# Kernel optimization log

Measured on AMD Instinct MI355X. Metric: run time of the kernel, lower is better.

## Reference

```python
import jax, jax.numpy as jnp
import numpy as np

B, T, D, S = 4, 8192, 512, 16

def setup_inputs() -> dict:
    key = jax.random.key(0)
    k1, k2, k3, k4, k5 = jax.random.split(key, 5)
    x = jax.random.normal(k1, (B, T, D), dtype=jnp.float32)
    # splat parameters as in __init__: centers ~ 0.02*randn, log_scales = 0
    centers = jax.random.normal(k2, (S, D), dtype=jnp.float32) * 0.02
    log_scales = jnp.zeros((S,), dtype=jnp.float32)
    # xavier-uniform linear weights (gain = 1/(1+layer_idx*0.1) = 1.0 for layer 0)
    limit = float(np.sqrt(6.0 / (D + D)))
    Wv = jax.random.uniform(k3, (D, D), minval=-limit, maxval=limit, dtype=jnp.float32)
    Wo = jax.random.uniform(k4, (D, D), minval=-limit, maxval=limit, dtype=jnp.float32)
    return {"x": x, "centers": centers, "log_scales": log_scales, "Wv": Wv, "Wo": Wo}

def reference(x, centers, log_scales, Wv, Wo):
    # scales clamped as in EnhancedAdaptiveSplat.get_scale
    scales = jnp.clip(jnp.exp(log_scales), 0.1, 2.0)           # [S]
    v = jnp.einsum('btd,ed->bte', x, Wv)                       # value projection [B,T,D]
    # squared distance token<->splat via expansion (no [B,T,S,D] intermediate)
    x2 = jnp.sum(x * x, axis=-1, keepdims=True)                # [B,T,1]
    c2 = jnp.sum(centers * centers, axis=-1)                   # [S]
    xc = jnp.einsum('btd,sd->bts', x, centers)                 # [B,T,S]
    d2 = x2 + c2 - 2.0 * xc                                    # [B,T,S]
    logits = -0.5 * d2 / (scales * scales)                     # gaussian kernel log-weights
    attn = jax.nn.softmax(logits, axis=-1)                     # normalize over splats [B,T,S]
    # tokens -> splats aggregation, then splats -> tokens distribution
    splat_states = jnp.einsum('bts,btd->bsd', attn, v)         # [B,S,D]
    out = jnp.einsum('bts,bsd->btd', attn, splat_states)       # [B,T,D]
    return jnp.einsum('btd,ed->bte', out, Wo)                  # output projection
```

## Files before the change

### kernel.cpp

```cpp
#include <hip/hip_runtime.h>
#include <hip/hip_bf16.h>
#include <math.h>

#define B_ 4
#define T_ 8192
#define D_ 512
#define S_ 16

#define CHUNK 64


typedef __attribute__((ext_vector_type(8))) short bf16x8;
typedef __attribute__((ext_vector_type(4))) float f32x4;

__device__ __forceinline__ float dot4(float4 a, float4 b) {
  return a.x * b.x + a.y * b.y + a.z * b.z + a.w * b.w;
}

__device__ __forceinline__ bf16x8 pack8(float4 a, float4 b) {
  union { __hip_bfloat162 h[4]; bf16x8 v; } u;
  u.h[0] = __float22bfloat162_rn(make_float2(a.x, a.y));
  u.h[1] = __float22bfloat162_rn(make_float2(a.z, a.w));
  u.h[2] = __float22bfloat162_rn(make_float2(b.x, b.y));
  u.h[3] = __float22bfloat162_rn(make_float2(b.z, b.w));
  return u.v;
}

__global__ __launch_bounds__(256, 2) void attn_ts_k(const float* __restrict__ x,
                                                    const float* __restrict__ centers,
                                                    const float* __restrict__ log_scales,
                                                    float* __restrict__ attn,
                                                    float* __restrict__ ts) {
  __shared__ __align__(16) float a_s[CHUNK][S_];
  const int lane = threadIdx.x & 63;
  const int w = threadIdx.x >> 6;
  const int g = lane >> 4;
  const int n = lane & 15;
  const int b = blockIdx.x >> 7;
  const int t0 = (blockIdx.x & 127) * CHUNK;
  const int tw = t0 + (w << 4);

  {
    bf16x8 cf[16];
    float c2p = 0.f;
    const float* crow = centers + n * D_ + (g << 3);
#pragma unroll
    for (int st = 0; st < 16; ++st) {
      float4 c0 = *(const float4*)(crow + st * 32);
      float4 c1 = *(const float4*)(crow + st * 32 + 4);
      c2p += dot4(c0, c0) + dot4(c1, c1);
      cf[st] = pack8(c0, c1);
    }
    c2p += __shfl_xor(c2p, 16, 64);
    c2p += __shfl_xor(c2p, 32, 64);

    const float sc = fminf(fmaxf(__expf(log_scales[n]), 0.1f), 2.0f);
    const float inv2 = 0.5f / (sc * sc);

    const float* xrow = x + ((size_t)b * T_ + tw + n) * D_ + (g << 3);
    f32x4 acc = {0.f, 0.f, 0.f, 0.f};
    float x2p = 0.f;
#pragma unroll
    for (int st = 0; st < 16; ++st) {
      float4 x0 = *(const float4*)(xrow + st * 32);
      float4 x1 = *(const float4*)(xrow + st * 32 + 4);
      x2p += dot4(x0, x0) + dot4(x1, x1);
      acc = __builtin_amdgcn_mfma_f32_16x16x32_bf16(pack8(x0, x1), cf[st], acc,
                                                    0, 0, 0);
    }
    x2p += __shfl_xor(x2p, 16, 64);
    x2p += __shfl_xor(x2p, 32, 64);

    float lg[4];
#pragma unroll
    for (int r = 0; r < 4; ++r) {
      float x2r = __shfl(x2p, (lane & 48) | ((g << 2) + r), 64);
      lg[r] = (2.f * acc[r] - x2r - c2p) * inv2;
    }

    float mx[4] = {lg[0], lg[1], lg[2], lg[3]};
#pragma unroll
    for (int dlt = 1; dlt < 16; dlt <<= 1)
#pragma unroll
      for (int r = 0; r < 4; ++r) mx[r] = fmaxf(mx[r], __shfl_xor(mx[r], dlt, 64));
    float ev[4], sm[4];
#pragma unroll
    for (int r = 0; r < 4; ++r) { ev[r] = __expf(lg[r] - mx[r]); sm[r] = ev[r]; }
#pragma unroll
    for (int dlt = 1; dlt < 16; dlt <<= 1)
#pragma unroll
      for (int r = 0; r < 4; ++r) sm[r] += __shfl_xor(sm[r], dlt, 64);

    float* ar = attn + ((size_t)b * T_ + tw) * S_;
#pragma unroll
    for (int r = 0; r < 4; ++r) {
      float av = ev[r] / sm[r];
      int trow = (g << 2) + r;
      ar[trow * S_ + n] = av;
      a_s[(w << 4) + trow][n] = av;
    }
  }

  __syncthreads();

  {
    const int d = threadIdx.x;
    float2 acc[S_];
#pragma unroll
    for (int si = 0; si < S_; ++si) acc[si] = make_float2(0.f, 0.f);

    const float* xb = x + ((size_t)b * T_ + t0) * D_;

#pragma unroll 8
    for (int t = 0; t < CHUNK; ++t) {
      float xv0 = xb[(size_t)t * D_ + d];
      float xv1 = xb[(size_t)t * D_ + d + 256];
      const float4* ap = (const float4*)a_s[t];
      float4 q0 = ap[0], q1 = ap[1], q2 = ap[2], q3 = ap[3];
      float av[S_] = {q0.x, q0.y, q0.z, q0.w, q1.x, q1.y, q1.z, q1.w,
                      q2.x, q2.y, q2.z, q2.w, q3.x, q3.y, q3.z, q3.w};
#pragma unroll
      for (int si = 0; si < S_; ++si) {
        acc[si].x += av[si] * xv0;
        acc[si].y += av[si] * xv1;
      }
    }

    float* tb = ts + (size_t)b * S_ * D_;
#pragma unroll
    for (int si = 0; si < S_; ++si) {
      atomicAdd(tb + si * D_ + d, acc[si].x);
      atomicAdd(tb + si * D_ + d + 256, acc[si].y);
    }
  }
}

__global__ __launch_bounds__(256) void proj_k(const float* __restrict__ in,
                                              const float* __restrict__ W,
                                              float* __restrict__ out) {
  __shared__ float red[4][64];
  const int r = blockIdx.x >> 3;
  const int eb = blockIdx.x & 7;
  const int el = threadIdx.x & 63;
  const int kc = threadIdx.x >> 6;
  const int e = (eb << 6) + el;

  const float4* w4 = (const float4*)(W + (size_t)e * D_ + kc * 128);
  const float4* i4 = (const float4*)(in + (size_t)r * D_ + kc * 128);
  float acc = 0.f;
#pragma unroll
  for (int k = 0; k < 32; ++k) acc += dot4(w4[k], i4[k]);

  red[kc][el] = acc;
  __syncthreads();
  if (kc == 0)
    out[(size_t)r * D_ + e] = red[0][el] + red[1][el] + red[2][el] + red[3][el];
}

#define K4_TOK 64
__global__ __launch_bounds__(256) void out_k(const float* __restrict__ attn,
                                             const float* __restrict__ ss_o,
                                             float* __restrict__ out) {
  const int chunks = T_ / K4_TOK;
  const int b = blockIdx.x / chunks;
  const int t0 = (blockIdx.x % chunks) * K4_TOK;
  const int w = threadIdx.x >> 6;
  const int lane = threadIdx.x & 63;
  const int e0 = (w << 7) + (lane << 1);

  float2 ssf[S_];
  const float* sb = ss_o + (size_t)b * S_ * D_;
#pragma unroll
  for (int s = 0; s < S_; ++s) ssf[s] = *(const float2*)(sb + s * D_ + e0);

  const float4* ab = (const float4*)(attn + ((size_t)b * T_ + t0) * S_);
  float* ob = out + ((size_t)b * T_ + t0) * D_ + e0;

#pragma unroll 4
  for (int t = 0; t < K4_TOK; ++t) {
    float4 a0 = ab[t * 4 + 0], a1 = ab[t * 4 + 1];
    float4 a2 = ab[t * 4 + 2], a3 = ab[t * 4 + 3];
    float av[S_] = {a0.x, a0.y, a0.z, a0.w, a1.x, a1.y, a1.z, a1.w,
                    a2.x, a2.y, a2.z, a2.w, a3.x, a3.y, a3.z, a3.w};
    float2 acc = make_float2(0.f, 0.f);
#pragma unroll
    for (int s = 0; s < S_; ++s) {
      acc.x += av[s] * ssf[s].x;
      acc.y += av[s] * ssf[s].y;
    }
    *(float2*)(ob + (size_t)t * D_) = acc;
  }
}

extern "C" void kernel_launch(void* const* d_in, const int* in_sizes, int n_in,
                              void* d_out, int out_size, void* d_ws, size_t ws_size,
                              hipStream_t stream) {
  const float* x          = (const float*)d_in[0];
  const float* centers    = (const float*)d_in[1];
  const float* log_scales = (const float*)d_in[2];
  const float* Wv         = (const float*)d_in[3];
  const float* Wo         = (const float*)d_in[4];
  float* out = (float*)d_out;

  float* attn = (float*)d_ws;
  float* ts   = attn + (size_t)B_ * T_ * S_;
  float* tmp  = ts + (size_t)B_ * S_ * D_;
  float* ss_o = tmp + (size_t)B_ * S_ * D_;

  hipMemsetAsync(ts, 0, (size_t)B_ * S_ * D_ * sizeof(float), stream);

  attn_ts_k<<<B_ * (T_ / CHUNK), 256, 0, stream>>>(x, centers, log_scales, attn, ts);
  proj_k<<<512, 256, 0, stream>>>(ts, Wv, tmp);
  proj_k<<<512, 256, 0, stream>>>(tmp, Wo, ss_o);
  out_k<<<B_ * (T_ / K4_TOK), 256, 0, stream>>>(attn, ss_o, out);
}
```

Measured before the change: 179.5 us.

## Halve token chunk, split D across wave pairs with LDS reduction

Token chunk per block drops from 64 to 32, doubling the grid of attn_ts_k and out_k. In attn_ts_k each 16-token tile is now computed by two waves, each covering half of D, and their MFMA partial sums plus norm partials are combined through shared memory before the softmax. Occupancy target rises to 4 blocks per SM. The aim is more parallelism and lower register pressure (no 16-entry cached center fragment), at the cost of an extra barrier, LDS traffic, idle waves during the softmax, and twice as many atomicAdds into ts.

```diff
diff --git a/kernel.cpp b/kernel.cpp
--- a/kernel.cpp
+++ b/kernel.cpp
@@ -7,7 +7,7 @@
 #define D_ 512
 #define S_ 16
 
-#define CHUNK 64
+#define CHUNK 32
 
 
 typedef __attribute__((ext_vector_type(8))) short bf16x8;
@@ -26,56 +26,69 @@
   return u.v;
 }
 
-__global__ __launch_bounds__(256, 2) void attn_ts_k(const float* __restrict__ x,
+__global__ __launch_bounds__(256, 4) void attn_ts_k(const float* __restrict__ x,
                                                     const float* __restrict__ centers,
                                                     const float* __restrict__ log_scales,
                                                     float* __restrict__ attn,
                                                     float* __restrict__ ts) {
   __shared__ __align__(16) float a_s[CHUNK][S_];
-  const int lane = threadIdx.x & 63;
-  const int w = threadIdx.x >> 6;
+  __shared__ float red[6][4][64];
+  const int tid = threadIdx.x;
+  const int lane = tid & 63;
+  const int w = tid >> 6;
   const int g = lane >> 4;
   const int n = lane & 15;
-  const int b = blockIdx.x >> 7;
-  const int t0 = (blockIdx.x & 127) * CHUNK;
-  const int tw = t0 + (w << 4);
+  const int b = blockIdx.x >> 8;
+  const int t0 = (blockIdx.x & 255) * CHUNK;
+  const int pair = w & 1;
+  const int half = w >> 1;
+  const int tw = t0 + (pair << 4);
 
   {
-    bf16x8 cf[16];
-    float c2p = 0.f;
-    const float* crow = centers + n * D_ + (g << 3);
-#pragma unroll
-    for (int st = 0; st < 16; ++st) {
+    const float* crow = centers + n * D_ + (half << 8) + (g << 3);
+    const float* xrow = x + ((size_t)b * T_ + tw + n) * D_ + (half << 8) + (g << 3);
+    f32x4 acc = {0.f, 0.f, 0.f, 0.f};
+    float x2p = 0.f, c2p = 0.f;
+#pragma unroll
+    for (int st = 0; st < 8; ++st) {
+      float4 x0 = *(const float4*)(xrow + st * 32);
+      float4 x1 = *(const float4*)(xrow + st * 32 + 4);
       float4 c0 = *(const float4*)(crow + st * 32);
       float4 c1 = *(const float4*)(crow + st * 32 + 4);
+      x2p += dot4(x0, x0) + dot4(x1, x1);
       c2p += dot4(c0, c0) + dot4(c1, c1);
-      cf[st] = pack8(c0, c1);
-    }
+      acc = __builtin_amdgcn_mfma_f32_16x16x32_bf16(pack8(x0, x1), pack8(c0, c1),
+                                                    acc, 0, 0, 0);
+    }
+    x2p += __shfl_xor(x2p, 16, 64);
+    x2p += __shfl_xor(x2p, 32, 64);
     c2p += __shfl_xor(c2p, 16, 64);
     c2p += __shfl_xor(c2p, 32, 64);
 
+    red[0][w][lane] = acc[0];
+    red[1][w][lane] = acc[1];
+    red[2][w][lane] = acc[2];
+    red[3][w][lane] = acc[3];
+    red[4][w][lane] = x2p;
+    red[5][w][lane] = c2p;
+  }
+  __syncthreads();
+
+  if (w < 2) {
+    float accr[4];
+#pragma unroll
+    for (int r = 0; r < 4; ++r) accr[r] = red[r][w][lane] + red[r][w + 2][lane];
+    float x2 = red[4][w][lane] + red[4][w + 2][lane];
+    float c2 = red[5][w][lane] + red[5][w + 2][lane];
+
     const float sc = fminf(fmaxf(__expf(log_scales[n]), 0.1f), 2.0f);
     const float inv2 = 0.5f / (sc * sc);
 
-    const float* xrow = x + ((size_t)b * T_ + tw + n) * D_ + (g << 3);
-    f32x4 acc = {0.f, 0.f, 0.f, 0.f};
-    float x2p = 0.f;
-#pragma unroll
-    for (int st = 0; st < 16; ++st) {
-      float4 x0 = *(const float4*)(xrow + st * 32);
-      float4 x1 = *(const float4*)(xrow + st * 32 + 4);
-      x2p += dot4(x0, x0) + dot4(x1, x1);
-      acc = __builtin_amdgcn_mfma_f32_16x16x32_bf16(pack8(x0, x1), cf[st], acc,
-                                                    0, 0, 0);
-    }
-    x2p += __shfl_xor(x2p, 16, 64);
-    x2p += __shfl_xor(x2p, 32, 64);
-
     float lg[4];
 #pragma unroll
     for (int r = 0; r < 4; ++r) {
-      float x2r = __shfl(x2p, (lane & 48) | ((g << 2) + r), 64);
-      lg[r] = (2.f * acc[r] - x2r - c2p) * inv2;
+      float x2r = __shfl(x2, (lane & 48) | ((g << 2) + r), 64);
+      lg[r] = (2.f * accr[r] - x2r - c2) * inv2;
     }
 
     float mx[4] = {lg[0], lg[1], lg[2], lg[3]};
@@ -97,14 +110,14 @@
       float av = ev[r] / sm[r];
       int trow = (g << 2) + r;
       ar[trow * S_ + n] = av;
-      a_s[(w << 4) + trow][n] = av;
+      a_s[(pair << 4) + trow][n] = av;
     }
   }
 
   __syncthreads();
 
   {
-    const int d = threadIdx.x;
+    const int d = tid;
     float2 acc[S_];
 #pragma unroll
     for (int si = 0; si < S_; ++si) acc[si] = make_float2(0.f, 0.f);
@@ -157,7 +170,7 @@
     out[(size_t)r * D_ + e] = red[0][el] + red[1][el] + red[2][el] + red[3][el];
 }
 
-#define K4_TOK 64
+#define K4_TOK 32
 __global__ __launch_bounds__(256) void out_k(const float* __restrict__ attn,
                                              const float* __restrict__ ss_o,
                                              float* __restrict__ out) {
```

New measurement: 184.0 us. 2.5% more time.
